# Performance work log

Measured on AMD Instinct MI355X. Metric: run time of the kernel, lower is better.

Reference implementation:

```python
import jax, jax.numpy as jnp
import numpy as np

# Grid constants from voxel_size=(0.2,0.2,4), point_cloud_range=(0,-40,-3,70.4,40,1)
VX, VY, VZ = 0.2, 0.2, 4.0
PCR = (0.0, -40.0, -3.0, 70.4, 40.0, 1.0)
NX, NY, NZ = 352, 400, 1   # round((hi-lo)/v) per axis
BATCH = 2
N_POINTS = 400000
CANVAS = BATCH * NZ * NY * NX  # dense canvas of all voxels (segment ids)
EPS = 1e-3  # BN1d eps from norm_cfg


def _vidx(coors):
    # linear voxel index: b*Z*Y*X + z*Y*X + y*X + x  (coors = [b,z,y,x])
    c = coors.astype(jnp.int32)
    return ((c[:, 0] * NZ + c[:, 1]) * NY + c[:, 2]) * NX + c[:, 3]


def _seg_mean(x, idx):
    # scatter-mean over voxels (DynamicScatter, average_points=True)
    s = jax.ops.segment_sum(x, idx, num_segments=CANVAS)
    c = jax.ops.segment_sum(jnp.ones((x.shape[0], 1), x.dtype), idx, num_segments=CANVAS)
    return s / jnp.maximum(c, 1.0)


def _seg_max(x, idx):
    # scatter-max over voxels (DynamicScatter, average_points=False); empty voxels -> 0
    m = jax.ops.segment_max(x, idx, num_segments=CANVAS)
    c = jax.ops.segment_sum(jnp.ones((x.shape[0],), x.dtype), idx, num_segments=CANVAS)
    return jnp.where((c > 0)[:, None], m, jnp.zeros_like(m))


def _bn_relu(x, g, b):
    # BN1d in training mode (batch stats, biased var), affine, then ReLU
    mu = x.mean(axis=0)
    var = x.var(axis=0)
    return jax.nn.relu((x - mu) * jax.lax.rsqrt(var + EPS) * g + b)


def setup_inputs() -> dict:
    key = jax.random.key(0)
    ks = jax.random.split(key, 6)
    features = jax.random.normal(ks[0], (N_POINTS, 4), jnp.float32)
    # coors [b, z, y, x]; batch column sorted so coors[-1,0]+1 == batch_size
    half = N_POINTS // 2
    b = jnp.concatenate([jnp.zeros(half, jnp.int32), jnp.ones(N_POINTS - half, jnp.int32)])
    z = jnp.zeros(N_POINTS, jnp.int32)  # NZ == 1
    y = jax.random.randint(ks[1], (N_POINTS,), 0, NY, jnp.int32)
    x = jax.random.randint(ks[2], (N_POINTS,), 0, NX, jnp.int32)
    coors = jnp.stack([b, z, y, x], axis=1)
    # VFE params: layer0 Linear(10->64, no bias), layer1 Linear(128->128, no bias)
    W0 = jax.random.normal(ks[3], (10, 64), jnp.float32) * 0.1
    g0 = jnp.ones((64,), jnp.float32)
    b0 = jnp.zeros((64,), jnp.float32)
    W1 = jax.random.normal(ks[4], (128, 128), jnp.float32) * 0.1
    g1 = jnp.ones((128,), jnp.float32)
    b1 = jnp.zeros((128,), jnp.float32)
    return {"features": features, "coors": coors, "W0": W0, "g0": g0, "b0": b0,
            "W1": W1, "g1": g1, "b1": b1}


def reference(features, coors, W0, g0, b0, W1, g1, b1):
    idx = _vidx(coors)
    # cluster center: scatter-mean of point features, gather back to points
    vmean = _seg_mean(features, idx)
    pts_mean = vmean[idx]
    f_cluster = features[:, :3] - pts_mean[:, :3]
    # voxel center offset
    cf = coors.astype(features.dtype)
    f_center = jnp.stack([
        features[:, 0] - (cf[:, 3] * VX + (VX / 2 + PCR[0])),
        features[:, 1] - (cf[:, 2] * VY + (VY / 2 + PCR[1])),
        features[:, 2] - (cf[:, 1] * VZ + (VZ / 2 + PCR[2])),
    ], axis=1)
    feat = jnp.concatenate([features, f_cluster, f_center], axis=1)  # (N, 10)
    # VFE layer 0 + voxel max pool + gather-broadcast + concat
    pf0 = _bn_relu(feat @ W0, g0, b0)           # (N, 64)
    v0 = _seg_max(pf0, idx)                     # (CANVAS, 64)
    feat1 = jnp.concatenate([pf0, v0[idx]], axis=1)  # (N, 128)
    # VFE layer 1 + final voxel max pool
    pf1 = _bn_relu(feat1 @ W1, g1, b1)          # (N, 128)
    voxel_feats = _seg_max(pf1, idx)            # (CANVAS, 128), dense canvas
    return voxel_feats
```

## Files before the change

kernel.cpp:

```cpp
#include <hip/hip_runtime.h>

#define NPTS 400000
#define NXv 352
#define NYv 400
#define CANVAS 281600
#define G2B 512
#define SCANB 275

typedef unsigned int uint;
typedef unsigned short ushort;
typedef __attribute__((ext_vector_type(8))) short short8;
typedef __attribute__((ext_vector_type(4))) float floatx4;

__device__ inline uint packbf(float a, float b) {
    uint ua = __float_as_uint(a);
    ua = (ua + 0x7fffu + ((ua >> 16) & 1u)) >> 16;
    uint ub = __float_as_uint(b);
    ub = (ub + 0x7fffu + ((ub >> 16) & 1u)) & 0xffff0000u;
    return ua | ub;
}
__device__ inline ushort bf16bits(float a) {
    uint u = __float_as_uint(a);
    return (ushort)((u + 0x7fffu + ((u >> 16) & 1u)) >> 16);
}
__device__ inline float lo16(uint u) { return __uint_as_float(u << 16); }
__device__ inline float hi16(uint u) { return __uint_as_float(u & 0xffff0000u); }
__device__ inline float bfval(ushort u) { return __uint_as_float(((uint)u) << 16); }

__device__ inline void gload_lds16(const uint* g, ushort* l) {
    __builtin_amdgcn_global_load_lds((const __attribute__((address_space(1))) void*)g,
                                     (__attribute__((address_space(3))) void*)l,
                                     16, 0, 0);
}

__global__ void k_bucket(const int4* __restrict__ coors, const float* __restrict__ W1,
                         int* __restrict__ idxbuf, int* __restrict__ pidx,
                         uint* __restrict__ ucnt, ushort* __restrict__ w1t) {
    int b = blockIdx.x;
    if (b < 1563) {
        int i = b * 256 + threadIdx.x;
        if (i >= NPTS) return;
        int4 c = coors[i];
        int idx = ((c.x + c.y) * NYv + c.z) * NXv + c.w;
        idxbuf[i] = idx;
        pidx[i] = (int)atomicAdd(&ucnt[idx], 1u);
    } else {
        int i = (b - 1563) * 256 + threadIdx.x;
        int n = i & 127, k = i >> 7;
        w1t[n * 128 + k] = bf16bits(W1[k * 128 + n]);
    }
}

__global__ __launch_bounds__(1024) void k_scanA(const uint* __restrict__ ucnt,
                                                uint* __restrict__ voff,
                                                uint* __restrict__ bsum) {
    __shared__ uint sh[1024];
    int t = threadIdx.x;
    int v = blockIdx.x * 1024 + t;
    uint val = ucnt[v];
    sh[t] = val;
    for (int off = 1; off < 1024; off <<= 1) {
        __syncthreads();
        uint x = (t >= off) ? sh[t - off] : 0u;
        __syncthreads();
        sh[t] += x;
    }
    uint incl = sh[t];
    voff[v] = incl - val;
    if (t == 1023) bsum[blockIdx.x] = incl;
}

__global__ __launch_bounds__(1024) void k_scanC(const uint* __restrict__ bsum,
                                                uint* __restrict__ voff) {
    __shared__ uint sh[1024];
    __shared__ uint bs[1024];
    int t = threadIdx.x;
    uint val = (t < SCANB) ? bsum[t] : 0u;
    sh[t] = val; bs[t] = val;
    for (int off = 1; off < 1024; off <<= 1) {
        __syncthreads();
        uint x = (t >= off) ? sh[t - off] : 0u;
        __syncthreads();
        sh[t] += x;
    }
    __syncthreads();
    uint off_ = sh[blockIdx.x] - bs[blockIdx.x];
    int v = blockIdx.x * 1024 + t;
    voff[v] += off_;
    if (blockIdx.x == SCANB - 1 && t == 1023) voff[CANVAS] = NPTS;
}

__global__ void k_perm(const int* __restrict__ idxbuf, const int* __restrict__ pidx,
                       const uint* __restrict__ voff, const float4* __restrict__ feat,
                       int* __restrict__ vidx, float4* __restrict__ featS) {
    int i = blockIdx.x * 256 + threadIdx.x;
    if (i >= NPTS) return;
    int idx = idxbuf[i];
    uint j = voff[idx] + (uint)pidx[i];
    vidx[j] = idx;
    featS[j] = feat[i];
}

__global__ void k_vmean(const float4* __restrict__ featS, const uint* __restrict__ voff,
                        float4* __restrict__ vmean) {
    int v = blockIdx.x * 256 + threadIdx.x;
    if (v >= CANVAS) return;
    uint s_ = voff[v], e_ = voff[v + 1];
    float4 s = make_float4(0.f, 0.f, 0.f, 0.f);
    for (uint j = s_; j < e_; ++j) {
        float4 f = featS[j];
        s.x += f.x; s.y += f.y; s.z += f.z; s.w += f.w;
    }
    float inv = 1.0f / (float)max((int)(e_ - s_), 1);
    vmean[v] = make_float4(s.x * inv, s.y * inv, s.z * inv, s.w * inv);
}

__global__ __launch_bounds__(256) void k_gemm1(
        const float4* __restrict__ featS, const int* __restrict__ vidx,
        const float4* __restrict__ vmean, const float* __restrict__ W0,
        uint* __restrict__ x0u, float* __restrict__ stats) {
    __shared__ float w0s[640];
    __shared__ __align__(8) ushort tile[256 * 68];
    __shared__ float ps[128], qs[128];
    for (int t = threadIdx.x; t < 640; t += 256) w0s[t] = W0[t];
    __syncthreads();
    int j = blockIdx.x * 256 + threadIdx.x;
    bool valid = j < NPTS;
    ushort* trow = &tile[threadIdx.x * 68];
    if (valid) {
        float4 f = featS[j];
        int idx = vidx[j];
        float4 vm = vmean[idx];
        int xq = idx % NXv;
        int yq = (idx / NXv) % NYv;
        float ft[10];
        ft[0] = f.x; ft[1] = f.y; ft[2] = f.z; ft[3] = f.w;
        ft[4] = f.x - vm.x;
        ft[5] = f.y - vm.y;
        ft[6] = f.z - vm.z;
        ft[7] = f.x - ((float)xq * 0.2f + 0.1f);
        ft[8] = f.y - ((float)yq * 0.2f - 39.9f);
        ft[9] = f.z + 1.0f;
        #pragma unroll
        for (int g = 0; g < 8; ++g) {
            float a[8];
            #pragma unroll
            for (int q = 0; q < 8; ++q) a[q] = 0.f;
            #pragma unroll
            for (int k = 0; k < 10; ++k) {
                float fk = ft[k];
                #pragma unroll
                for (int q = 0; q < 8; ++q) a[q] = fmaf(fk, w0s[k * 64 + g * 8 + q], a[q]);
            }
            uint4 w;
            w.x = packbf(a[0], a[1]); w.y = packbf(a[2], a[3]);
            w.z = packbf(a[4], a[5]); w.w = packbf(a[6], a[7]);
            ((uint2*)trow)[g * 2 + 0] = make_uint2(w.x, w.y);
            ((uint2*)trow)[g * 2 + 1] = make_uint2(w.z, w.w);
        }
    } else {
        #pragma unroll
        for (int g = 0; g < 16; ++g) ((uint2*)trow)[g] = make_uint2(0u, 0u);
    }
    __syncthreads();

    int base = blockIdx.x * 256;
    for (int i = threadIdx.x; i < 4096; i += 256) {
        int r = i >> 4, ch = i & 15;
        if (base + r < NPTS) {
            uint2 u = *(const uint2*)&tile[r * 68 + ch * 4];
            *(uint2*)(x0u + (size_t)(base + r) * 32 + ch * 2) = u;
        }
    }

    if (threadIdx.x < 128) {
        int c = threadIdx.x & 63, half = threadIdx.x >> 6;
        float s = 0.f, q = 0.f;
        for (int r = half * 128; r < half * 128 + 128; ++r) {
            float xv = bfval(tile[r * 68 + c]);
            s += xv;
            q = fmaf(xv, xv, q);
        }
        ps[half * 64 + c] = s;
        qs[half * 64 + c] = q;
    }
    __syncthreads();
    if (threadIdx.x < 64) {
        int c = threadIdx.x;
        atomicAdd(&stats[c], ps[c] + ps[64 + c]);
        atomicAdd(&stats[64 + c], qs[c] + qs[64 + c]);
    }
}

__global__ void k_vmax0(const uint* __restrict__ x0u, const uint* __restrict__ voff,
                        const float* __restrict__ stats, const float* __restrict__ g0,
                        const float* __restrict__ b0, uint* __restrict__ v0u,
                        uint* __restrict__ x0b) {
    __shared__ float s[128];
    if (threadIdx.x < 64) {
        int c = threadIdx.x;
        float mu = stats[c] * (1.0f / NPTS);
        float var = stats[64 + c] * (1.0f / NPTS) - mu * mu;
        float sc = (1.0f / sqrtf(var + 1e-3f)) * g0[c];
        s[c] = sc;
        s[64 + c] = fmaf(-mu, sc, b0[c]);
    }
    __syncthreads();
    int t = blockIdx.x * 256 + threadIdx.x;
    int v = t >> 4;
    if (v >= CANVAS) return;
    uint s_ = voff[v], e_ = voff[v + 1];
    if (s_ == e_) return;
    int c = (t & 15) << 2;
    float4 m = make_float4(0.f, 0.f, 0.f, 0.f);
    for (uint j = s_; j < e_; ++j) {
        uint2 u = *(const uint2*)(x0u + (size_t)j * 32 + (c >> 1));
        float a = fmaxf(fmaf(lo16(u.x), s[c + 0], s[64 + c + 0]), 0.f);
        float b = fmaxf(fmaf(hi16(u.x), s[c + 1], s[64 + c + 1]), 0.f);
        float cc = fmaxf(fmaf(lo16(u.y), s[c + 2], s[64 + c + 2]), 0.f);
        float d = fmaxf(fmaf(hi16(u.y), s[c + 3], s[64 + c + 3]), 0.f);
        m.x = fmaxf(m.x, a); m.y = fmaxf(m.y, b);
        m.z = fmaxf(m.z, cc); m.w = fmaxf(m.w, d);
        uint2 o2; o2.x = packbf(a, b); o2.y = packbf(cc, d);
        *(uint2*)(x0b + (size_t)j * 32 + (c >> 1)) = o2;
    }
    uint2 o; o.x = packbf(m.x, m.y); o.y = packbf(m.z, m.w);
    *(uint2*)(v0u + (size_t)v * 32 + (c >> 1)) = o;
}

__global__ __launch_bounds__(256) void k_gemm2p(
        const uint* __restrict__ x0b, const uint* __restrict__ v0u,
        const int* __restrict__ vidx, const uint* __restrict__ voff,
        const ushort* __restrict__ w1t,
        ushort* __restrict__ vmaxc, float* __restrict__ sums) {
    __shared__ __align__(16) ushort As[2 * 64 * 128];
    __shared__ __align__(8) ushort CsT[128 * 74];
    __shared__ int svid[2][64];

    int lane = threadIdx.x & 63, wid = threadIdx.x >> 6;
    int m = lane & 15, q = lane >> 4;

    short8 breg[8][4];
    #pragma unroll
    for (int ct = 0; ct < 8; ++ct) {
        const ushort* br = &w1t[(ct * 16 + m) * 128 + q * 8];
        #pragma unroll
        for (int ks = 0; ks < 4; ++ks)
            breg[ct][ks] = *(const short8*)&br[ks * 32];
    }

    int p0 = (int)((long long)blockIdx.x * NPTS / G2B);
    int p1 = (int)((long long)(blockIdx.x + 1) * NPTS / G2B);
    int ps, pe;
    { int v = vidx[p0]; ps = (voff[v] == (uint)p0) ? p0 : (int)voff[v + 1]; }
    if (p1 >= NPTS) pe = NPTS;
    else { int v = vidx[p1]; pe = (voff[v] == (uint)p1) ? p1 : (int)voff[v + 1]; }

    float run = -3.0e38f, csum = 0.f, csq = 0.f;
    int vcur = -1;

    auto stageM = [&](int r0s, int bufn) {
        int nrows = min(64, pe - r0s);
        for (int i = threadIdx.x; i < 1024; i += 128) {
            int r = i >> 4, ch = i & 15;
            uint4 u = make_uint4(0u, 0u, 0u, 0u);
            if (r < nrows) {
                const uint* srcp = (ch < 8)
                    ? (x0b + (size_t)(r0s + r) * 32 + ch * 4)
                    : (v0u + (size_t)vidx[r0s + r] * 32 + (ch - 8) * 4);
                u = *(const uint4*)srcp;
            }
            *(uint4*)&As[bufn * 8192 + r * 128 + ch * 8] = u;
        }
    };
    auto stageDMA = [&](int r0n, int bufn) {
        int j0 = wid * 8;
        #pragma unroll
        for (int j = j0; j < j0 + 8; ++j) {
            int rl = j * 4 + (lane >> 4);
            int p = lane & 15;
            int vr = svid[bufn][rl];
            const uint* s32 = (p < 8)
                ? (x0b + (size_t)(r0n + rl) * 32 + p * 4)
                : (v0u + (size_t)vr * 32 + (p - 8) * 4);
            gload_lds16(s32, &As[bufn * 8192 + j * 512]);
        }
    };

    if (threadIdx.x < 64) {
        int nr0 = (ps < pe) ? min(64, pe - ps) : 0;
        svid[0][threadIdx.x] = (threadIdx.x < nr0) ? vidx[ps + threadIdx.x] : -1;
    }
    if (threadIdx.x < 128 && ps < pe) stageM(ps, 0);
    __syncthreads();

    int sp = 0;
    for (int r0 = ps; r0 < pe; r0 += 64, sp ^= 1) {
        int spn = sp ^ 1;
        bool hasnext = (r0 + 64 < pe);
        int vn = -1;
        if (hasnext && threadIdx.x < 64) {
            int rn = r0 + 64 + threadIdx.x;
            if (rn < pe) vn = vidx[rn];
        }
        const ushort* ab = &As[sp * 8192 + (wid * 16 + m) * 128 + q * 8];
        short8 a0 = *(const short8*)&ab[0];
        short8 a1 = *(const short8*)&ab[32];
        short8 a2 = *(const short8*)&ab[64];
        short8 a3 = *(const short8*)&ab[96];
        #pragma unroll
        for (int ct = 0; ct < 8; ++ct) {
            floatx4 acc = {0.f, 0.f, 0.f, 0.f};
            acc = __builtin_amdgcn_mfma_f32_16x16x32_bf16(a0, breg[ct][0], acc, 0, 0, 0);
            acc = __builtin_amdgcn_mfma_f32_16x16x32_bf16(a1, breg[ct][1], acc, 0, 0, 0);
            acc = __builtin_amdgcn_mfma_f32_16x16x32_bf16(a2, breg[ct][2], acc, 0, 0, 0);
            acc = __builtin_amdgcn_mfma_f32_16x16x32_bf16(a3, breg[ct][3], acc, 0, 0, 0);
            uint* cp = (uint*)&CsT[(ct * 16 + m) * 74 + wid * 16 + q * 4];
            cp[0] = packbf(acc[0], acc[1]);
            cp[1] = packbf(acc[2], acc[3]);
        }
        if (hasnext && threadIdx.x < 64) svid[spn][threadIdx.x] = vn;
        __syncthreads();

        if (threadIdx.x < 128) {
            if (hasnext) {
                if (r0 + 128 <= pe) stageDMA(r0 + 64, spn);
                else stageM(r0 + 64, spn);
            }
            asm volatile("s_waitcnt vmcnt(0)" ::: "memory");
        } else {
            int c = threadIdx.x - 128;
            const uint* crow = (const uint*)&CsT[c * 74];
            #pragma unroll 4
            for (int rp = 0; rp < 32; ++rp) {
                uint u = crow[rp];
                int va = svid[sp][2 * rp], vb = svid[sp][2 * rp + 1];
                float xa = lo16(u), xb = hi16(u);
                bool brk = (va != vcur);
                if (brk && vcur >= 0) vmaxc[(size_t)vcur * 128 + c] = bf16bits(run);
                run = brk ? xa : fmaxf(run, xa);
                vcur = va;
                csum += xa; csq = fmaf(xa, xa, csq);
                brk = (vb != vcur);
                if (brk && vcur >= 0) vmaxc[(size_t)vcur * 128 + c] = bf16bits(run);
                run = brk ? xb : fmaxf(run, xb);
                vcur = vb;
                csum += xb; csq = fmaf(xb, xb, csq);
            }
        }
        __syncthreads();
    }

    if (threadIdx.x >= 128) {
        int c = threadIdx.x - 128;
        if (vcur >= 0) vmaxc[(size_t)vcur * 128 + c] = bf16bits(run);
        atomicAdd(&sums[c], csum);
        atomicAdd(&sums[128 + c], csq);
    }
}

__global__ __launch_bounds__(256) void k_bnout(const ushort* __restrict__ vmaxc,
        const uint* __restrict__ voff, const float* __restrict__ stats,
        const float* __restrict__ g1, const float* __restrict__ b1,
        float4* __restrict__ out) {
    __shared__ float s[256];
    if (threadIdx.x < 128) {
        int c = threadIdx.x;
        float mu = stats[128 + c] * (1.0f / NPTS);
        float var = stats[256 + c] * (1.0f / NPTS) - mu * mu;
        float sc = (1.0f / sqrtf(var + 1e-3f)) * g1[c];
        s[c] = sc;
        s[128 + c] = fmaf(-mu, sc, b1[c]);
    }
    __syncthreads();
    int t = blockIdx.x * 256 + threadIdx.x;
    int v = t >> 5;
    if (v >= CANVAS) return;
    int c = (t & 31) << 2;
    float4 m = make_float4(0.f, 0.f, 0.f, 0.f);
    if (voff[v + 1] != voff[v]) {
        uint2 u = *(const uint2*)(vmaxc + (size_t)v * 128 + c);
        m.x = fmaxf(fmaf(lo16(u.x), s[c + 0], s[128 + c + 0]), 0.f);
        m.y = fmaxf(fmaf(hi16(u.x), s[c + 1], s[128 + c + 1]), 0.f);
        m.z = fmaxf(fmaf(lo16(u.y), s[c + 2], s[128 + c + 2]), 0.f);
        m.w = fmaxf(fmaf(hi16(u.y), s[c + 3], s[128 + c + 3]), 0.f);
    }
    out[(size_t)v * 32 + (c >> 2)] = m;
}

extern "C" void kernel_launch(void* const* d_in, const int* in_sizes, int n_in,
                              void* d_out, int out_size, void* d_ws, size_t ws_size,
                              hipStream_t stream) {
    const float4* feat  = (const float4*)d_in[0];
    const int4*   coors = (const int4*)d_in[1];
    const float*  W0    = (const float*)d_in[2];
    const float*  g0    = (const float*)d_in[3];
    const float*  b0    = (const float*)d_in[4];
    const float*  W1    = (const float*)d_in[5];
    const float*  g1    = (const float*)d_in[6];
    const float*  b1    = (const float*)d_in[7];

    char* ws = (char*)d_ws;
    int*    idxbuf = (int*)(ws + 0);
    int*    pidx   = (int*)(ws + 1600000);
    uint*   ucnt   = (uint*)(ws + 3200000);
    float*  stats  = (float*)(ws + 4326400);
    uint*   voff   = (uint*)(ws + 4329472);
    uint*   bsum   = (uint*)(ws + 5455888);
    int*    vidx   = (int*)(ws + 5459984);
    float*  featS  = (float*)(ws + 7059984);
    float*  vmean  = (float*)(ws + 13459984);
    ushort* w1t    = (ushort*)(ws + 17965584);
    uint*   x0u    = (uint*)(ws + 17998352);
    uint*   v0u    = (uint*)(ws + 69198352);
    ushort* vmaxc  = (ushort*)(ws + 105243152);
    uint*   x0b    = (uint*)(ws + 177332752);

    hipMemsetAsync(ws + 3200000, 0, 1129472, stream);

    const int BLK = 256;
    int gpts = (NPTS + BLK - 1) / BLK;
    int gvox = (CANVAS + BLK - 1) / BLK;

    k_bucket<<<gpts + 64, BLK, 0, stream>>>(coors, W1, idxbuf, pidx, ucnt, w1t);
    k_scanA<<<SCANB, 1024, 0, stream>>>(ucnt, voff, bsum);
    k_scanC<<<SCANB, 1024, 0, stream>>>(bsum, voff);
    k_perm<<<gpts, BLK, 0, stream>>>(idxbuf, pidx, voff, feat, vidx, (float4*)featS);
    k_vmean<<<gvox, BLK, 0, stream>>>((const float4*)featS, voff, (float4*)vmean);
    k_gemm1<<<gpts, BLK, 0, stream>>>((const float4*)featS, vidx, (const float4*)vmean,
                                      W0, x0u, stats);
    k_vmax0<<<CANVAS * 16 / BLK, BLK, 0, stream>>>(x0u, voff, stats, g0, b0, v0u, x0b);
    k_gemm2p<<<G2B, BLK, 0, stream>>>(x0b, v0u, vidx, voff, w1t, vmaxc, stats + 128);
    k_bnout<<<CANVAS * 32 / BLK, BLK, 0, stream>>>(vmaxc, voff, stats, g1, b1,
                                                   (float4*)d_out);
}
```

Baseline: 453.4 us.

## Swizzle A tile in LDS and accumulate BN stats from fp32 MFMA outputs

The A-tile staging (both the manual path and the direct global-to-LDS path) now XOR-swizzles 16-byte chunks by row, and the MFMA fragment loads read with the matching swizzle. The intent is to remove LDS bank conflicts on the short8 reads. BN sum and sum-of-squares are now accumulated per wave in registers from the fp32 accumulators, rather than from bf16-rounded values in the serial segment-max loop. They are reduced with shuffles and LDS before the atomics. This lightens the post-processing loop but adds 16 registers per thread and extra barriers at the end of the kernel.

```diff
diff --git a/kernel.cpp b/kernel.cpp
--- a/kernel.cpp
+++ b/kernel.cpp
@@ -239,6 +239,7 @@
 
     int lane = threadIdx.x & 63, wid = threadIdx.x >> 6;
     int m = lane & 15, q = lane >> 4;
+    int mm = m & 7;
 
     short8 breg[8][4];
     #pragma unroll
@@ -256,8 +257,11 @@
     if (p1 >= NPTS) pe = NPTS;
     else { int v = vidx[p1]; pe = (voff[v] == (uint)p1) ? p1 : (int)voff[v + 1]; }
 
-    float run = -3.0e38f, csum = 0.f, csq = 0.f;
+    float run = -3.0e38f;
     int vcur = -1;
+    float csum[8], csq[8];
+    #pragma unroll
+    for (int k = 0; k < 8; ++k) { csum[k] = 0.f; csq[k] = 0.f; }
 
     auto stageM = [&](int r0s, int bufn) {
         int nrows = min(64, pe - r0s);
@@ -270,7 +274,7 @@
                     : (v0u + (size_t)vidx[r0s + r] * 32 + (ch - 8) * 4);
                 u = *(const uint4*)srcp;
             }
-            *(uint4*)&As[bufn * 8192 + r * 128 + ch * 8] = u;
+            *(uint4*)&As[bufn * 8192 + r * 128 + ((ch ^ (r & 7)) * 8)] = u;
         }
     };
     auto stageDMA = [&](int r0n, int bufn) {
@@ -279,10 +283,11 @@
         for (int j = j0; j < j0 + 8; ++j) {
             int rl = j * 4 + (lane >> 4);
             int p = lane & 15;
+            int pl = p ^ (rl & 7);
             int vr = svid[bufn][rl];
-            const uint* s32 = (p < 8)
-                ? (x0b + (size_t)(r0n + rl) * 32 + p * 4)
-                : (v0u + (size_t)vr * 32 + (p - 8) * 4);
+            const uint* s32 = (pl < 8)
+                ? (x0b + (size_t)(r0n + rl) * 32 + pl * 4)
+                : (v0u + (size_t)vr * 32 + (pl - 8) * 4);
             gload_lds16(s32, &As[bufn * 8192 + j * 512]);
         }
     };
@@ -303,11 +308,11 @@
             int rn = r0 + 64 + threadIdx.x;
             if (rn < pe) vn = vidx[rn];
         }
-        const ushort* ab = &As[sp * 8192 + (wid * 16 + m) * 128 + q * 8];
-        short8 a0 = *(const short8*)&ab[0];
-        short8 a1 = *(const short8*)&ab[32];
-        short8 a2 = *(const short8*)&ab[64];
-        short8 a3 = *(const short8*)&ab[96];
+        const ushort* rowp = &As[sp * 8192 + (wid * 16 + m) * 128];
+        short8 a0 = *(const short8*)&rowp[((q + 0) ^ mm) * 8];
+        short8 a1 = *(const short8*)&rowp[((q + 4) ^ mm) * 8];
+        short8 a2 = *(const short8*)&rowp[((q + 8) ^ mm) * 8];
+        short8 a3 = *(const short8*)&rowp[((q + 12) ^ mm) * 8];
         #pragma unroll
         for (int ct = 0; ct < 8; ++ct) {
             floatx4 acc = {0.f, 0.f, 0.f, 0.f};
@@ -315,6 +320,11 @@
             acc = __builtin_amdgcn_mfma_f32_16x16x32_bf16(a1, breg[ct][1], acc, 0, 0, 0);
             acc = __builtin_amdgcn_mfma_f32_16x16x32_bf16(a2, breg[ct][2], acc, 0, 0, 0);
             acc = __builtin_amdgcn_mfma_f32_16x16x32_bf16(a3, breg[ct][3], acc, 0, 0, 0);
+            #pragma unroll
+            for (int rg = 0; rg < 4; ++rg) {
+                csum[ct] += acc[rg];
+                csq[ct] = fmaf(acc[rg], acc[rg], csq[ct]);
+            }
             uint* cp = (uint*)&CsT[(ct * 16 + m) * 74 + wid * 16 + q * 4];
             cp[0] = packbf(acc[0], acc[1]);
             cp[1] = packbf(acc[2], acc[3]);
@@ -340,12 +350,10 @@
                 if (brk && vcur >= 0) vmaxc[(size_t)vcur * 128 + c] = bf16bits(run);
                 run = brk ? xa : fmaxf(run, xa);
                 vcur = va;
-                csum += xa; csq = fmaf(xa, xa, csq);
                 brk = (vb != vcur);
                 if (brk && vcur >= 0) vmaxc[(size_t)vcur * 128 + c] = bf16bits(run);
                 run = brk ? xb : fmaxf(run, xb);
                 vcur = vb;
-                csum += xb; csq = fmaf(xb, xb, csq);
             }
         }
         __syncthreads();
@@ -354,8 +362,36 @@
     if (threadIdx.x >= 128) {
         int c = threadIdx.x - 128;
         if (vcur >= 0) vmaxc[(size_t)vcur * 128 + c] = bf16bits(run);
-        atomicAdd(&sums[c], csum);
-        atomicAdd(&sums[128 + c], csq);
+    }
+
+    float* red = (float*)As;
+    #pragma unroll
+    for (int k = 0; k < 8; ++k) {
+        csum[k] += __shfl_xor(csum[k], 16);
+        csum[k] += __shfl_xor(csum[k], 32);
+        csq[k]  += __shfl_xor(csq[k], 16);
+        csq[k]  += __shfl_xor(csq[k], 32);
+    }
+    if (lane < 16) {
+        #pragma unroll
+        for (int ct = 0; ct < 8; ++ct) red[wid * 128 + ct * 16 + lane] = csum[ct];
+    }
+    __syncthreads();
+    if (threadIdx.x < 128) {
+        float t = red[threadIdx.x] + red[128 + threadIdx.x]
+                + red[256 + threadIdx.x] + red[384 + threadIdx.x];
+        atomicAdd(&sums[threadIdx.x], t);
+    }
+    __syncthreads();
+    if (lane < 16) {
+        #pragma unroll
+        for (int ct = 0; ct < 8; ++ct) red[wid * 128 + ct * 16 + lane] = csq[ct];
+    }
+    __syncthreads();
+    if (threadIdx.x < 128) {
+        float t = red[threadIdx.x] + red[128 + threadIdx.x]
+                + red[256 + threadIdx.x] + red[384 + threadIdx.x];
+        atomicAdd(&sums[128 + threadIdx.x], t);
     }
 }
 
```

Result: slower. 504.2 us (+11.2%).
